# Optimization experiments

Hardware: AMD Instinct MI355X
Metric: run time of the kernel (lower is better)

Reference implementation:

```python
import jax, jax.numpy as jnp
import numpy as np

B, T, D_MODEL, N_HEADS = 2, 2048, 1024, 16
HEAD_DIM = D_MODEL // N_HEADS
EPS = 1e-6
ROPE_BASE = 10000.0


def _rope_cos_sin(seq_len, dim, offset=0, dtype=jnp.float32):
    half = dim // 2
    inv_freq = 1.0 / (ROPE_BASE ** (jnp.arange(half, dtype=jnp.float32) / half))
    pos = jnp.arange(offset, offset + seq_len, dtype=jnp.float32)
    freqs = pos[:, None] * inv_freq[None, :]              # (T, half)
    emb = jnp.concatenate([freqs, freqs], axis=-1)        # (T, dim)
    return jnp.cos(emb).astype(dtype), jnp.sin(emb).astype(dtype)


def _rotate_half(x):
    x1, x2 = jnp.split(x, 2, axis=-1)
    return jnp.concatenate([-x2, x1], axis=-1)


def setup_inputs() -> dict:
    key = jax.random.key(0)
    k1, k2, k3 = jax.random.split(key, 3)
    x = jax.random.normal(k1, (B, T, D_MODEL), dtype=jnp.float32)
    norm_w = jnp.ones((D_MODEL,), dtype=jnp.float32)
    w_qkv = jax.random.normal(k2, (3 * D_MODEL, D_MODEL), dtype=jnp.float32) * 0.02
    w_out = jax.random.normal(k3, (D_MODEL, D_MODEL), dtype=jnp.float32) * 0.02
    return {"x": x, "norm_w": norm_w, "w_qkv": w_qkv, "w_out": w_out}


def reference(x, norm_w, w_qkv, w_out):
    # RMSNorm (pre-norm)
    h = x * jax.lax.rsqrt(jnp.mean(jnp.square(x), axis=-1, keepdims=True) + EPS) * norm_w
    # Fused QKV projection: (B,T,3*D)
    qkv = jnp.einsum('btd,ed->bte', h, w_qkv).reshape(B, T, 3, N_HEADS, HEAD_DIM)
    q, k, v = qkv[:, :, 0], qkv[:, :, 1], qkv[:, :, 2]   # each (B,T,H,Dh)
    # RoPE on q, k (offset=0)
    cos, sin = _rope_cos_sin(T, HEAD_DIM, dtype=q.dtype)
    cos = cos[None, :, None, :]
    sin = sin[None, :, None, :]
    q = q * cos + _rotate_half(q) * sin
    k = k * cos + _rotate_half(k) * sin
    # Causal scaled dot-product attention
    scale = 1.0 / np.sqrt(HEAD_DIM)
    scores = jnp.einsum('bqhd,bkhd->bhqk', q, k) * scale  # (B,H,T,T)
    causal = jnp.tril(jnp.ones((T, T), dtype=bool))
    scores = jnp.where(causal[None, None], scores, jnp.finfo(scores.dtype).min)
    attn = jax.nn.softmax(scores, axis=-1)
    out = jnp.einsum('bhqk,bkhd->bqhd', attn, v).reshape(B, T, D_MODEL)
    out = jnp.einsum('btd,ed->bte', out, w_out)
    return x + out
```

## Files before the change

kernel.cpp:

```cpp
#include <hip/hip_runtime.h>
#include <math.h>

typedef unsigned short u16;
typedef unsigned int u32;
typedef __attribute__((ext_vector_type(4))) float f32x4;
typedef __attribute__((ext_vector_type(8))) short s16x8;

#define GLL16(g, l) __builtin_amdgcn_global_load_lds( \
    (const __attribute__((address_space(1))) void*)(g), \
    (__attribute__((address_space(3))) void*)(l), 16, 0, 0)

__device__ __forceinline__ u16 f2bf(float f) {
  union { float f; u32 u; } v; v.f = f;
  u32 r = v.u + 0x7FFFu + ((v.u >> 16) & 1u);
  return (u16)(r >> 16);
}
__device__ __forceinline__ float bf2f(u16 h) {
  union { u32 u; float f; } v; v.u = ((u32)h) << 16;
  return v.f;
}
__device__ __forceinline__ u32 pk2bf(float lo, float hi) {
  union { float f; u32 u; } a, b; a.f = lo; b.f = hi;
  return __builtin_amdgcn_perm(b.u + 0x8000u, a.u + 0x8000u, 0x07060302u);
}
__device__ __forceinline__ float fexp2(float x) {
#if __has_builtin(__builtin_amdgcn_exp2f)
  return __builtin_amdgcn_exp2f(x);
#else
  return exp2f(x);
#endif
}

__global__ __launch_bounds__(256) void cast_kernel(const float* __restrict__ src,
                                                   u16* __restrict__ dst, int n4) {
  int i = blockIdx.x * 256 + threadIdx.x;
  if (i >= n4) return;
  float4 v = ((const float4*)src)[i];
  uint2 o;
  o.x = (u32)f2bf(v.x) | ((u32)f2bf(v.y) << 16);
  o.y = (u32)f2bf(v.z) | ((u32)f2bf(v.w) << 16);
  ((uint2*)dst)[i] = o;
}

__global__ __launch_bounds__(256) void rmsnorm_kernel(const float* __restrict__ x,
                                                      const float* __restrict__ wgt,
                                                      u16* __restrict__ h) {
  const int row = blockIdx.x, tid = threadIdx.x;
  const float4 v = *(const float4*)&x[(size_t)row * 1024 + tid * 4];
  float ss = v.x * v.x + v.y * v.y + v.z * v.z + v.w * v.w;
  ss += __shfl_xor(ss, 1);  ss += __shfl_xor(ss, 2);  ss += __shfl_xor(ss, 4);
  ss += __shfl_xor(ss, 8);  ss += __shfl_xor(ss, 16); ss += __shfl_xor(ss, 32);
  __shared__ float red[4];
  if ((tid & 63) == 0) red[tid >> 6] = ss;
  __syncthreads();
  const float tot = red[0] + red[1] + red[2] + red[3];
  const float s = rsqrtf(tot * (1.0f / 1024.0f) + 1e-6f);
  const float4 g = *(const float4*)&wgt[tid * 4];
  uint2 o;
  o.x = (u32)f2bf(v.x * s * g.x) | ((u32)f2bf(v.y * s * g.y) << 16);
  o.y = (u32)f2bf(v.z * s * g.z) | ((u32)f2bf(v.w * s * g.w) << 16);
  *(uint2*)&h[(size_t)row * 1024 + tid * 4] = o;
}

template <int EPI>
__global__ __launch_bounds__(256) void gemm_bt(const u16* __restrict__ A,
                                               const u16* __restrict__ Bt,
                                               u16* __restrict__ Cb,
                                               float* __restrict__ Cf,
                                               const float* __restrict__ resid,
                                               int M, int N, int K) {
  __shared__ __attribute__((aligned(16))) u16 As[128 * 32];
  __shared__ __attribute__((aligned(16))) u16 Bs[128 * 32];
  const int tid = threadIdx.x;
  const int w = tid >> 6, lane = tid & 63;
  const int quad = lane >> 4, l16 = lane & 15;
  const int gm0 = blockIdx.y * 128, gn0 = blockIdx.x * 128;
  const int wm = (w & 1) * 64, wn = (w >> 1) * 64;

  f32x4 acc[4][4] = {};

  for (int k0 = 0; k0 < K; k0 += 32) {
    __syncthreads();
    if (w < 2) {
      #pragma unroll
      for (int i = 0; i < 4; ++i) {
        int sb = (w * 4 + i) * 64;
        int slot = sb + lane;
        int m = slot >> 2, c = (slot & 3) ^ (m & 3);
        GLL16(A + (size_t)(gm0 + m) * K + k0 + c * 8, &As[sb * 8]);
      }
    } else {
      #pragma unroll
      for (int i = 0; i < 4; ++i) {
        int sb = ((w - 2) * 4 + i) * 64;
        int slot = sb + lane;
        int n = slot >> 2, c = (slot & 3) ^ (n & 3);
        GLL16(Bt + (size_t)(gn0 + n) * K + k0 + c * 8, &Bs[sb * 8]);
      }
    }
    __syncthreads();
    s16x8 aF[4], bF[4];
    #pragma unroll
    for (int i = 0; i < 4; ++i) {
      int m = wm + i * 16 + l16;
      aF[i] = *(const s16x8*)&As[(m * 4 + (quad ^ (m & 3))) * 8];
    }
    #pragma unroll
    for (int j = 0; j < 4; ++j) {
      int n = wn + j * 16 + l16;
      bF[j] = *(const s16x8*)&Bs[(n * 4 + (quad ^ (n & 3))) * 8];
    }
    #pragma unroll
    for (int i = 0; i < 4; ++i)
      #pragma unroll
      for (int j = 0; j < 4; ++j)
        acc[i][j] = __builtin_amdgcn_mfma_f32_16x16x32_bf16(aF[i], bF[j], acc[i][j], 0, 0, 0);
  }

  #pragma unroll
  for (int i = 0; i < 4; ++i) {
    int row0 = gm0 + wm + i * 16 + quad * 4;
    #pragma unroll
    for (int j = 0; j < 4; ++j) {
      int col = gn0 + wn + j * 16 + l16;
      #pragma unroll
      for (int r = 0; r < 4; ++r) {
        size_t idx = (size_t)(row0 + r) * N + col;
        if (EPI == 0) Cb[idx] = f2bf(acc[i][j][r]);
        else          Cf[idx] = acc[i][j][r] + resid[idx];
      }
    }
  }
}

__global__ __launch_bounds__(256) void rope_kernel(const u16* __restrict__ qkv,
                                                   u16* __restrict__ Qr,
                                                   u16* __restrict__ Kr,
                                                   u16* __restrict__ Vt) {
  const int tt = blockIdx.x, bh = blockIdx.y;
  const int b = bh >> 4, h = bh & 15;
  const int tid = threadIdx.x;
  const float QSCALE = 0.125f * 1.4426950408889634f;

  #pragma unroll
  for (int ii = 0; ii < 8; ++ii) {
    int idx = ii * 256 + tid;
    int tl = idx >> 5, jj = idx & 31;
    int t = tt * 64 + tl;
    size_t mrow = (size_t)(b * 2048 + t) * 3072 + h * 64;
    float q1 = bf2f(qkv[mrow + jj]),        q2 = bf2f(qkv[mrow + 32 + jj]);
    float k1 = bf2f(qkv[mrow + 1024 + jj]), k2 = bf2f(qkv[mrow + 1024 + 32 + jj]);
    float invf = exp2f(-(float)jj * (13.287712379549449f / 32.0f));
    float ang = (float)t * invf;
    float sn, cs;
    sincosf(ang, &sn, &cs);
    size_t orow = (size_t)(bh * 2048 + t) * 64;
    Qr[orow + jj]      = f2bf((q1 * cs - q2 * sn) * QSCALE);
    Qr[orow + 32 + jj] = f2bf((q2 * cs + q1 * sn) * QSCALE);
    Kr[orow + jj]      = f2bf(k1 * cs - k2 * sn);
    Kr[orow + 32 + jj] = f2bf(k2 * cs + k1 * sn);
  }

  __shared__ __attribute__((aligned(16))) u16 Vl[64][72];
  for (int s = tid; s < 512; s += 256) {
    int r = s >> 3, c8 = (s & 7) * 8;
    *(uint4*)&Vl[r][c8] =
        *(const uint4*)&qkv[(size_t)(b * 2048 + tt * 64 + r) * 3072 + 2048 + h * 64 + c8];
  }
  __syncthreads();
  for (int s = tid; s < 512; s += 256) {
    int d = s >> 3, t8 = (s & 7) * 8;
    u16 tmp[8];
    #pragma unroll
    for (int k = 0; k < 8; ++k) tmp[k] = Vl[t8 + k][d];
    *(uint4*)&Vt[(size_t)(bh * 64 + d) * 2048 + tt * 64 + t8] = *(uint4*)tmp;
  }
}

__global__ __launch_bounds__(512) void attn_kernel(const u16* __restrict__ Qr,
                                                   const u16* __restrict__ Kr,
                                                   const u16* __restrict__ Vt,
                                                   u16* __restrict__ AO) {
  __shared__ __attribute__((aligned(16))) char smem[102400];
  const int tid = threadIdx.x;
  const int w = tid >> 6, lane = tid & 63;
  const int wq = w & 3, wp = w >> 2;
  const int quad = lane >> 4, l16 = lane & 15;
  const int id = blockIdx.x;
  const int bh = id & 31;
  const int c  = id >> 5;
  const int b = bh >> 4, h = bh & 15;
  const size_t qkb = (size_t)bh * (2048 * 64);
  const size_t vtb = (size_t)bh * (64 * 2048);
  u16* Pw = (u16*)(smem + 65536 + w * 4608);

  const int srow = lane >> 3;
  const int scg  = (lane & 7) ^ srow;
  const int smat = w & 1, stp = (w >> 1) & 1, shalf = (w >> 2) & 1;

  auto STAGE = [&](int j0, int d) {
    const int jn = j0 + stp;
    if (smat == 0) {
      #pragma unroll
      for (int ii = 0; ii < 4; ++ii) {
        int i = shalf * 4 + ii;
        GLL16(Kr + qkb + (size_t)(jn * 64 + i * 8 + srow) * 64 + scg * 8,
              smem + (stp * 2 + d) * 8192 + i * 1024);
      }
    } else {
      #pragma unroll
      for (int ii = 0; ii < 4; ++ii) {
        int i = shalf * 4 + ii;
        GLL16(Vt + vtb + (size_t)(i * 8 + srow) * 2048 + jn * 64 + scg * 8,
              smem + 32768 + (stp * 2 + d) * 8192 + i * 1024);
      }
    }
  };

  for (int t = 0; t < 2; ++t) {
    const int qblk = t ? (15 - c) : c;
    const int q0w = qblk * 128 + wq * 32;
    const int steps = qblk + 1;

    s16x8 bQ[2][2];
    #pragma unroll
    for (int s = 0; s < 2; ++s)
      #pragma unroll
      for (int hf = 0; hf < 2; ++hf)
        bQ[s][hf] = *(const s16x8*)&Qr[qkb + (size_t)(q0w + s * 16 + l16) * 64 + hf * 32 + quad * 8];

    f32x4 O[2][4] = {};
    float l_run[2] = {0.0f, 0.0f};

    STAGE(0, 0);
    __syncthreads();

    for (int st = 0; st < steps; ++st) {
      const int cur = st & 1;
      if (st + 1 < steps) STAGE(2 * st + 2, cur ^ 1);

      const int j = 2 * st + wp;
      if (j * 64 <= q0w + 31) {
        const u16* Kb = (const u16*)(smem + (wp * 2 + cur) * 8192);
        const u16* Vb = (const u16*)(smem + 32768 + (wp * 2 + cur) * 8192);
        const bool masked = (j * 64 + 63 > q0w);
        const int rsw = (l16 & 7);

        s16x8 aK[4][2];
        #pragma unroll
        for (int kt = 0; kt < 4; ++kt)
          #pragma unroll
          for (int hf = 0; hf < 2; ++hf)
            aK[kt][hf] = *(const s16x8*)&Kb[(kt * 16 + l16) * 64 + (((hf * 4 + quad) ^ rsw) * 8)];

        f32x4 S[2][4];
        __builtin_amdgcn_s_setprio(1);
        #pragma unroll
        for (int kt = 0; kt < 4; ++kt)
          #pragma unroll
          for (int s = 0; s < 2; ++s) {
            f32x4 z = {};
            z = __builtin_amdgcn_mfma_f32_16x16x32_bf16(aK[kt][0], bQ[s][0], z, 0, 0, 0);
            S[s][kt] = __builtin_amdgcn_mfma_f32_16x16x32_bf16(aK[kt][1], bQ[s][1], z, 0, 0, 0);
          }
        __builtin_amdgcn_s_setprio(0);

        if (masked) {
          #pragma unroll
          for (int s = 0; s < 2; ++s) {
            int q = q0w + s * 16 + l16;
            #pragma unroll
            for (int kt = 0; kt < 4; ++kt) {
              int key0 = j * 64 + kt * 16 + quad * 4;
              #pragma unroll
              for (int r = 0; r < 4; ++r)
                if (key0 + r > q) S[s][kt][r] = -1e30f;
            }
          }
        }

        #pragma unroll
        for (int s = 0; s < 2; ++s) {
          float sum = 0.0f;
          #pragma unroll
          for (int kt = 0; kt < 4; ++kt) {
            #pragma unroll
            for (int r = 0; r < 4; ++r) {
              float e = fexp2(S[s][kt][r]);
              S[s][kt][r] = e;
              sum += e;
            }
          }
          sum += __shfl_xor(sum, 16);
          sum += __shfl_xor(sum, 32);
          l_run[s] += sum;
          #pragma unroll
          for (int kt = 0; kt < 4; ++kt) {
            uint2 pw;
            pw.x = pk2bf(S[s][kt][0], S[s][kt][1]);
            pw.y = pk2bf(S[s][kt][2], S[s][kt][3]);
            *(uint2*)&Pw[s * 1152 + l16 * 72 + kt * 16 + quad * 4] = pw;
          }
        }

        s16x8 bP[2][2];
        #pragma unroll
        for (int s = 0; s < 2; ++s) {
          bP[s][0] = *(const s16x8*)&Pw[s * 1152 + l16 * 72 + quad * 8];
          bP[s][1] = *(const s16x8*)&Pw[s * 1152 + l16 * 72 + 32 + quad * 8];
        }
        s16x8 aV[4][2];
        #pragma unroll
        for (int dt = 0; dt < 4; ++dt)
          #pragma unroll
          for (int hf = 0; hf < 2; ++hf)
            aV[dt][hf] = *(const s16x8*)&Vb[(dt * 16 + l16) * 64 + (((hf * 4 + quad) ^ rsw) * 8)];

        __builtin_amdgcn_s_setprio(1);
        #pragma unroll
        for (int dt = 0; dt < 4; ++dt)
          #pragma unroll
          for (int s = 0; s < 2; ++s) {
            O[s][dt] = __builtin_amdgcn_mfma_f32_16x16x32_bf16(aV[dt][0], bP[s][0], O[s][dt], 0, 0, 0);
            O[s][dt] = __builtin_amdgcn_mfma_f32_16x16x32_bf16(aV[dt][1], bP[s][1], O[s][dt], 0, 0, 0);
          }
        __builtin_amdgcn_s_setprio(0);
      }

      __syncthreads();
    }

    if (wp == 1) {
      float* Lsl = (float*)(smem + 65536 + wq * 512);
      Lsl[lane]      = l_run[0];
      Lsl[64 + lane] = l_run[1];
      f32x4* slot = (f32x4*)smem + wq * 512;
      #pragma unroll
      for (int s = 0; s < 2; ++s)
        #pragma unroll
        for (int dt = 0; dt < 4; ++dt)
          slot[(s * 4 + dt) * 64 + lane] = O[s][dt];
    }
    __syncthreads();
    if (wp == 0) {
      const float* Lsl = (const float*)(smem + 65536 + wq * 512);
      const f32x4* slot = (const f32x4*)smem + wq * 512;
      #pragma unroll
      for (int s = 0; s < 2; ++s) {
        float l_tot = l_run[s] + Lsl[s * 64 + lane];
        float inv = __builtin_amdgcn_rcpf(l_tot);
        int q = q0w + s * 16 + l16;
        #pragma unroll
        for (int dt = 0; dt < 4; ++dt) {
          f32x4 o = O[s][dt] + slot[(s * 4 + dt) * 64 + lane];
          uint2 ow;
          ow.x = pk2bf(o[0] * inv, o[1] * inv);
          ow.y = pk2bf(o[2] * inv, o[3] * inv);
          *(uint2*)&AO[(size_t)(b * 2048 + q) * 1024 + h * 64 + dt * 16 + quad * 4] = ow;
        }
      }
    }
    __syncthreads();
  }
}

extern "C" void kernel_launch(void* const* d_in, const int* in_sizes, int n_in,
                              void* d_out, int out_size, void* d_ws, size_t ws_size,
                              hipStream_t stream) {
  const float* x      = (const float*)d_in[0];
  const float* norm_w = (const float*)d_in[1];
  const float* w_qkv  = (const float*)d_in[2];
  const float* w_out  = (const float*)d_in[3];
  float* out = (float*)d_out;

  u16* ws     = (u16*)d_ws;
  u16* wqkv_b = ws;
  u16* wout_b = wqkv_b + 3145728;
  u16* h_b    = wout_b + 1048576;
  u16* qkv_b  = h_b + 4194304;
  u16* Qr     = qkv_b + 12582912;
  u16* Kr     = Qr + 4194304;
  u16* Vt     = Kr + 4194304;
  u16* AO     = Vt + 4194304;

  cast_kernel<<<3072, 256, 0, stream>>>(w_qkv, wqkv_b, 786432);
  cast_kernel<<<1024, 256, 0, stream>>>(w_out, wout_b, 262144);
  rmsnorm_kernel<<<4096, 256, 0, stream>>>(x, norm_w, h_b);
  gemm_bt<0><<<dim3(24, 32), 256, 0, stream>>>(h_b, wqkv_b, qkv_b, nullptr, nullptr,
                                               4096, 3072, 1024);
  rope_kernel<<<dim3(32, 32), 256, 0, stream>>>(qkv_b, Qr, Kr, Vt);
  attn_kernel<<<256, 512, 0, stream>>>(Qr, Kr, Vt, AO);
  gemm_bt<1><<<dim3(8, 32), 256, 0, stream>>>(AO, wout_b, nullptr, out, x,
                                              4096, 1024, 1024);
}
```

Measured before the change: 190.8 us.

## Add 256x256 pipelined QKV GEMM and merge prep kernels into one launch

Replaces the 128x128 QKV projection GEMM with a 512-thread, 256x256-tile kernel. It uses double-buffered direct global-to-LDS loads, interleaves quarter-tile MFMA phases with staging of the next K slices, and applies block-index swizzling for L2 locality. Separately, the two weight casts and the RMSNorm are merged into one prep kernel to cut launch count. The larger tile raises operand reuse per LDS load, but leaves only 192 blocks for the GPU's CUs and relies on hand-placed waitcnt and barriers that are fragile to get right.

```diff
diff --git a/kernel.cpp b/kernel.cpp
--- a/kernel.cpp
+++ b/kernel.cpp
@@ -9,6 +9,8 @@
 #define GLL16(g, l) __builtin_amdgcn_global_load_lds( \
     (const __attribute__((address_space(1))) void*)(g), \
     (__attribute__((address_space(3))) void*)(l), 16, 0, 0)
+
+#define MFMA16(a, b, c) __builtin_amdgcn_mfma_f32_16x16x32_bf16(a, b, c, 0, 0, 0)
 
 __device__ __forceinline__ u16 f2bf(float f) {
   union { float f; u32 u; } v; v.f = f;
@@ -31,35 +33,45 @@
 #endif
 }
 
-__global__ __launch_bounds__(256) void cast_kernel(const float* __restrict__ src,
-                                                   u16* __restrict__ dst, int n4) {
-  int i = blockIdx.x * 256 + threadIdx.x;
-  if (i >= n4) return;
-  float4 v = ((const float4*)src)[i];
-  uint2 o;
-  o.x = (u32)f2bf(v.x) | ((u32)f2bf(v.y) << 16);
-  o.y = (u32)f2bf(v.z) | ((u32)f2bf(v.w) << 16);
-  ((uint2*)dst)[i] = o;
-}
-
-__global__ __launch_bounds__(256) void rmsnorm_kernel(const float* __restrict__ x,
-                                                      const float* __restrict__ wgt,
-                                                      u16* __restrict__ h) {
-  const int row = blockIdx.x, tid = threadIdx.x;
-  const float4 v = *(const float4*)&x[(size_t)row * 1024 + tid * 4];
-  float ss = v.x * v.x + v.y * v.y + v.z * v.z + v.w * v.w;
-  ss += __shfl_xor(ss, 1);  ss += __shfl_xor(ss, 2);  ss += __shfl_xor(ss, 4);
-  ss += __shfl_xor(ss, 8);  ss += __shfl_xor(ss, 16); ss += __shfl_xor(ss, 32);
+__global__ __launch_bounds__(256) void prep_kernel(const float* __restrict__ x,
+                                                   const float* __restrict__ wgt,
+                                                   const float* __restrict__ w_qkv,
+                                                   const float* __restrict__ w_out,
+                                                   u16* __restrict__ h,
+                                                   u16* __restrict__ wqkv_b,
+                                                   u16* __restrict__ wout_b) {
   __shared__ float red[4];
-  if ((tid & 63) == 0) red[tid >> 6] = ss;
-  __syncthreads();
-  const float tot = red[0] + red[1] + red[2] + red[3];
-  const float s = rsqrtf(tot * (1.0f / 1024.0f) + 1e-6f);
-  const float4 g = *(const float4*)&wgt[tid * 4];
-  uint2 o;
-  o.x = (u32)f2bf(v.x * s * g.x) | ((u32)f2bf(v.y * s * g.y) << 16);
-  o.y = (u32)f2bf(v.z * s * g.z) | ((u32)f2bf(v.w * s * g.w) << 16);
-  *(uint2*)&h[(size_t)row * 1024 + tid * 4] = o;
+  const int bid = blockIdx.x, tid = threadIdx.x;
+  if (bid < 4096) {
+    const int row = bid;
+    const float4 v = *(const float4*)&x[(size_t)row * 1024 + tid * 4];
+    float ss = v.x * v.x + v.y * v.y + v.z * v.z + v.w * v.w;
+    ss += __shfl_xor(ss, 1);  ss += __shfl_xor(ss, 2);  ss += __shfl_xor(ss, 4);
+    ss += __shfl_xor(ss, 8);  ss += __shfl_xor(ss, 16); ss += __shfl_xor(ss, 32);
+    if ((tid & 63) == 0) red[tid >> 6] = ss;
+    __syncthreads();
+    const float tot = red[0] + red[1] + red[2] + red[3];
+    const float s = rsqrtf(tot * (1.0f / 1024.0f) + 1e-6f);
+    const float4 g = *(const float4*)&wgt[tid * 4];
+    uint2 o;
+    o.x = (u32)f2bf(v.x * s * g.x) | ((u32)f2bf(v.y * s * g.y) << 16);
+    o.y = (u32)f2bf(v.z * s * g.z) | ((u32)f2bf(v.w * s * g.w) << 16);
+    *(uint2*)&h[(size_t)row * 1024 + tid * 4] = o;
+  } else if (bid < 7168) {
+    int i = (bid - 4096) * 256 + tid;
+    float4 v = ((const float4*)w_qkv)[i];
+    uint2 o;
+    o.x = (u32)f2bf(v.x) | ((u32)f2bf(v.y) << 16);
+    o.y = (u32)f2bf(v.z) | ((u32)f2bf(v.w) << 16);
+    ((uint2*)wqkv_b)[i] = o;
+  } else {
+    int i = (bid - 7168) * 256 + tid;
+    float4 v = ((const float4*)w_out)[i];
+    uint2 o;
+    o.x = (u32)f2bf(v.x) | ((u32)f2bf(v.y) << 16);
+    o.y = (u32)f2bf(v.z) | ((u32)f2bf(v.w) << 16);
+    ((uint2*)wout_b)[i] = o;
+  }
 }
 
 template <int EPI>
@@ -114,7 +126,7 @@
     for (int i = 0; i < 4; ++i)
       #pragma unroll
       for (int j = 0; j < 4; ++j)
-        acc[i][j] = __builtin_amdgcn_mfma_f32_16x16x32_bf16(aF[i], bF[j], acc[i][j], 0, 0, 0);
+        acc[i][j] = MFMA16(aF[i], bF[j], acc[i][j]);
   }
 
   #pragma unroll
@@ -129,6 +141,149 @@
         if (EPI == 0) Cb[idx] = f2bf(acc[i][j][r]);
         else          Cf[idx] = acc[i][j][r] + resid[idx];
       }
+    }
+  }
+}
+
+__global__ __launch_bounds__(512) void gemm256(const u16* __restrict__ A,
+                                               const u16* __restrict__ Bt,
+                                               u16* __restrict__ Cb) {
+  __shared__ __attribute__((aligned(16))) char smem[131072];
+  const int tid = threadIdx.x;
+  const int w = tid >> 6, lane = tid & 63;
+  const int quad = lane >> 4, l16 = lane & 15;
+  const int wr = w >> 2, wc = w & 3;
+  const int rsw = l16 & 7;
+  const int id = blockIdx.x;
+  const int sw = (id & 7) * 24 + (id >> 3);
+  const int by = sw / 12, bx = sw - by * 12;
+  const int gm0 = by * 256, gn0 = bx * 256;
+  const int scg = (lane & 7) ^ (lane >> 3);
+
+  auto STAGE_HALF = [&](int kt, int part) {
+    const int sb = (kt & 1) * 65536 + (part >> 1) * 32768 + (part & 1) * 16384;
+    const u16* src = (part >> 1) ? Bt : A;
+    const int g0 = ((part >> 1) ? gn0 : gm0) + (part & 1) * 128;
+    const int k0 = kt * 64;
+    #pragma unroll
+    for (int q = 0; q < 2; ++q) {
+      int r = q * 64 + (tid >> 3);
+      GLL16(src + (size_t)(g0 + r) * 1024 + k0 + scg * 8,
+            smem + sb + q * 8192 + w * 1024);
+    }
+  };
+
+  f32x4 acc[8][4] = {};
+
+  #pragma unroll
+  for (int n = 0; n < 8; ++n) STAGE_HALF(n >> 2, n & 3);
+  __syncthreads();
+
+  for (int kt = 0; kt < 16; ++kt) {
+    const char* Ab = smem + (kt & 1) * 65536;
+    const char* Bb = Ab + 32768;
+    const int arow = wr * 128 + l16;
+    const int brow = wc * 64 + l16;
+    s16x8 aA[4][2], bB[4][2];
+
+    #pragma unroll
+    for (int fi = 0; fi < 4; ++fi) {
+      const char* p = Ab + (arow + fi * 16) * 128;
+      aA[fi][0] = *(const s16x8*)(p + ((quad ^ rsw) * 16));
+      aA[fi][1] = *(const s16x8*)(p + (((4 + quad) ^ rsw) * 16));
+    }
+    #pragma unroll
+    for (int fj = 0; fj < 2; ++fj) {
+      const char* p = Bb + (brow + fj * 16) * 128;
+      bB[fj][0] = *(const s16x8*)(p + ((quad ^ rsw) * 16));
+      bB[fj][1] = *(const s16x8*)(p + (((4 + quad) ^ rsw) * 16));
+    }
+    if (kt >= 1 && kt < 15) STAGE_HALF(kt + 1, 0);
+    __builtin_amdgcn_s_barrier();
+    asm volatile("s_waitcnt lgkmcnt(0)" ::: "memory");
+    __builtin_amdgcn_sched_barrier(0);
+    __builtin_amdgcn_s_setprio(1);
+    #pragma unroll
+    for (int fi = 0; fi < 4; ++fi)
+      #pragma unroll
+      for (int fj = 0; fj < 2; ++fj) {
+        acc[fi][fj] = MFMA16(aA[fi][0], bB[fj][0], acc[fi][fj]);
+        acc[fi][fj] = MFMA16(aA[fi][1], bB[fj][1], acc[fi][fj]);
+      }
+    __builtin_amdgcn_s_setprio(0);
+    __builtin_amdgcn_s_barrier();
+    asm volatile("" ::: "memory");
+
+    #pragma unroll
+    for (int fj = 0; fj < 2; ++fj) {
+      const char* p = Bb + (brow + (2 + fj) * 16) * 128;
+      bB[2 + fj][0] = *(const s16x8*)(p + ((quad ^ rsw) * 16));
+      bB[2 + fj][1] = *(const s16x8*)(p + (((4 + quad) ^ rsw) * 16));
+    }
+    if (kt >= 1 && kt < 15) STAGE_HALF(kt + 1, 1);
+    __builtin_amdgcn_s_barrier();
+    asm volatile("s_waitcnt lgkmcnt(0)" ::: "memory");
+    __builtin_amdgcn_sched_barrier(0);
+    __builtin_amdgcn_s_setprio(1);
+    #pragma unroll
+    for (int fi = 0; fi < 4; ++fi)
+      #pragma unroll
+      for (int fj = 0; fj < 2; ++fj) {
+        acc[fi][2 + fj] = MFMA16(aA[fi][0], bB[2 + fj][0], acc[fi][2 + fj]);
+        acc[fi][2 + fj] = MFMA16(aA[fi][1], bB[2 + fj][1], acc[fi][2 + fj]);
+      }
+    __builtin_amdgcn_s_setprio(0);
+    __builtin_amdgcn_s_barrier();
+    asm volatile("" ::: "memory");
+
+    #pragma unroll
+    for (int fi = 0; fi < 4; ++fi) {
+      const char* p = Ab + (arow + (4 + fi) * 16) * 128;
+      aA[fi][0] = *(const s16x8*)(p + ((quad ^ rsw) * 16));
+      aA[fi][1] = *(const s16x8*)(p + (((4 + quad) ^ rsw) * 16));
+    }
+    if (kt < 14) STAGE_HALF(kt + 2, 2);
+    __builtin_amdgcn_s_barrier();
+    asm volatile("s_waitcnt lgkmcnt(0)" ::: "memory");
+    __builtin_amdgcn_sched_barrier(0);
+    __builtin_amdgcn_s_setprio(1);
+    #pragma unroll
+    for (int fi = 0; fi < 4; ++fi)
+      #pragma unroll
+      for (int fj = 0; fj < 2; ++fj) {
+        acc[4 + fi][fj] = MFMA16(aA[fi][0], bB[fj][0], acc[4 + fi][fj]);
+        acc[4 + fi][fj] = MFMA16(aA[fi][1], bB[fj][1], acc[4 + fi][fj]);
+      }
+    __builtin_amdgcn_s_setprio(0);
+    __builtin_amdgcn_s_barrier();
+    asm volatile("" ::: "memory");
+
+    if (kt < 14) STAGE_HALF(kt + 2, 3);
+    __builtin_amdgcn_s_barrier();
+    __builtin_amdgcn_s_setprio(1);
+    #pragma unroll
+    for (int fi = 0; fi < 4; ++fi)
+      #pragma unroll
+      for (int fj = 0; fj < 2; ++fj) {
+        acc[4 + fi][2 + fj] = MFMA16(aA[fi][0], bB[2 + fj][0], acc[4 + fi][2 + fj]);
+        acc[4 + fi][2 + fj] = MFMA16(aA[fi][1], bB[2 + fj][1], acc[4 + fi][2 + fj]);
+      }
+    __builtin_amdgcn_s_setprio(0);
+    if (kt < 14)      asm volatile("s_waitcnt vmcnt(4)" ::: "memory");
+    else if (kt < 15) asm volatile("s_waitcnt vmcnt(0)" ::: "memory");
+    __builtin_amdgcn_s_barrier();
+    asm volatile("" ::: "memory");
+  }
+
+  #pragma unroll
+  for (int g = 0; g < 8; ++g) {
+    const int row0 = gm0 + wr * 128 + g * 16 + quad * 4;
+    #pragma unroll
+    for (int fj = 0; fj < 4; ++fj) {
+      const int col = gn0 + wc * 64 + fj * 16 + l16;
+      #pragma unroll
+      for (int r = 0; r < 4; ++r)
+        Cb[(size_t)(row0 + r) * 3072 + col] = f2bf(acc[g][fj][r]);
     }
   }
 }
@@ -260,8 +415,8 @@
           #pragma unroll
           for (int s = 0; s < 2; ++s) {
             f32x4 z = {};
-            z = __builtin_amdgcn_mfma_f32_16x16x32_bf16(aK[kt][0], bQ[s][0], z, 0, 0, 0);
-            S[s][kt] = __builtin_amdgcn_mfma_f32_16x16x32_bf16(aK[kt][1], bQ[s][1], z, 0, 0, 0);
+            z = MFMA16(aK[kt][0], bQ[s][0], z);
+            S[s][kt] = MFMA16(aK[kt][1], bQ[s][1], z);
           }
         __builtin_amdgcn_s_setprio(0);
 
@@ -321,8 +476,8 @@
         for (int dt = 0; dt < 4; ++dt)
           #pragma unroll
           for (int s = 0; s < 2; ++s) {
-            O[s][dt] = __builtin_amdgcn_mfma_f32_16x16x32_bf16(aV[dt][0], bP[s][0], O[s][dt], 0, 0, 0);
-            O[s][dt] = __builtin_amdgcn_mfma_f32_16x16x32_bf16(aV[dt][1], bP[s][1], O[s][dt], 0, 0, 0);
+            O[s][dt] = MFMA16(aV[dt][0], bP[s][0], O[s][dt]);
+            O[s][dt] = MFMA16(aV[dt][1], bP[s][1], O[s][dt]);
           }
         __builtin_amdgcn_s_setprio(0);
       }
@@ -383,11 +538,8 @@
   u16* Vt     = Kr + 4194304;
   u16* AO     = Vt + 4194304;
 
-  cast_kernel<<<3072, 256, 0, stream>>>(w_qkv, wqkv_b, 786432);
-  cast_kernel<<<1024, 256, 0, stream>>>(w_out, wout_b, 262144);
-  rmsnorm_kernel<<<4096, 256, 0, stream>>>(x, norm_w, h_b);
-  gemm_bt<0><<<dim3(24, 32), 256, 0, stream>>>(h_b, wqkv_b, qkv_b, nullptr, nullptr,
-                                               4096, 3072, 1024);
+  prep_kernel<<<8192, 256, 0, stream>>>(x, norm_w, w_qkv, w_out, h_b, wqkv_b, wout_b);
+  gemm256<<<192, 512, 0, stream>>>(h_b, wqkv_b, qkv_b);
   rope_kernel<<<dim3(32, 32), 256, 0, stream>>>(qkv_b, Qr, Kr, Vt);
   attn_kernel<<<256, 512, 0, stream>>>(Qr, Kr, Vt, AO);
   gemm_bt<1><<<dim3(8, 32), 256, 0, stream>>>(AO, wout_b, nullptr, out, x,
```

Result: faster. 186.0 us (-2.5%).
